# Optimization experiments

Hardware: AMD Instinct MI355X
Metric: run time of the kernel (lower is better)

## Reference

```python
import jax, jax.numpy as jnp
import numpy as np
from jax import lax

WINDOW_SIZE = 11
GAUSSIAN_SIGMA = 1.5
CROP_BORDER = 4
C1 = (0.01 * 255.0) ** 2
C2 = (0.03 * 255.0) ** 2


def _gaussian_kernel_window(ws: int, sigma: float) -> jnp.ndarray:
    # matches cv2.getGaussianKernel(ws, sigma) outer product
    x = jnp.arange(ws, dtype=jnp.float32) - (ws - 1) / 2.0
    g = jnp.exp(-(x ** 2) / (2.0 * sigma ** 2))
    g = g / jnp.sum(g)
    return jnp.outer(g, g)  # [ws, ws]


def _depthwise_conv(x: jnp.ndarray, kern: jnp.ndarray) -> jnp.ndarray:
    # x: [N, C, H, W]; kern: [C, 1, ws, ws]; valid padding, stride 1, groups=C
    return lax.conv_general_dilated(
        x, kern, window_strides=(1, 1), padding='VALID',
        dimension_numbers=('NCHW', 'OIHW', 'NCHW'),
        feature_group_count=x.shape[1])


def setup_inputs() -> dict:
    key = jax.random.key(0)
    k1, k2 = jax.random.split(key)
    raw_tensor = jax.random.uniform(k1, (32, 3, 512, 512), dtype=jnp.float32)
    dst_tensor = jax.random.uniform(k2, (32, 3, 512, 512), dtype=jnp.float32)
    return {"raw_tensor": raw_tensor, "dst_tensor": dst_tensor}


def reference(raw_tensor, dst_tensor):
    cb = CROP_BORDER
    raw = raw_tensor[:, :, cb:-cb, cb:-cb] * 255.0
    dst = dst_tensor[:, :, cb:-cb, cb:-cb] * 255.0
    C = raw.shape[1]
    kern = jnp.broadcast_to(
        _gaussian_kernel_window(WINDOW_SIZE, GAUSSIAN_SIGMA)[None, None],
        (C, 1, WINDOW_SIZE, WINDOW_SIZE)).astype(raw.dtype)

    raw_mean = _depthwise_conv(raw, kern)
    dst_mean = _depthwise_conv(dst, kern)
    raw_mean_sq = raw_mean ** 2
    dst_mean_sq = dst_mean ** 2
    raw_dst_mean = raw_mean * dst_mean
    raw_var = _depthwise_conv(raw * raw, kern) - raw_mean_sq
    dst_var = _depthwise_conv(dst * dst, kern) - dst_mean_sq
    raw_dst_cov = _depthwise_conv(raw * dst, kern) - raw_dst_mean

    num = (2.0 * raw_dst_mean + C1) * (2.0 * raw_dst_cov + C2)
    den = (raw_mean_sq + dst_mean_sq + C1) * (raw_var + dst_var + C2)
    ssim_map = num / den
    return jnp.mean(ssim_map, axis=(1, 2, 3)).astype(jnp.float32)  # [B]
```

## Files before the change

### kernel.cpp

```cpp
#include <hip/hip_runtime.h>


#define IMG   512
#define OUTD  494
#define CB    4
#define TW    64
#define TH    26
#define VSW   76
#define C1F   6.5025f
#define C2F   58.5225f
#define NPIX  732108.0f
#define XBLK  8
#define YBLK  19
#define SLOTS 456

__global__ __launch_bounds__(256, 4) void ssim_main(
        const float* __restrict__ raw, const float* __restrict__ dst,
        float* __restrict__ partial) {
    __shared__ float vs[4][TH][VSW];
    __shared__ float red[4];

    const int tid = threadIdx.x;
    const int bc  = blockIdx.z;
    const int b   = bc / 3;
    const int c3  = bc - b * 3;
    const int ty0 = blockIdx.y * TH;
    const int tx0 = blockIdx.x * TW;

    float gw[11];
    {
        float s = 0.f;
        #pragma unroll
        for (int k = 0; k < 11; ++k) {
            float x = (float)(k - 5);
            gw[k] = expf(-x * x * (1.0f / 4.5f));
            s += gw[k];
        }
        float inv = 1.0f / s;
        #pragma unroll
        for (int k = 0; k < 11; ++k) gw[k] *= inv;
    }

    const float* rb = raw + (size_t)bc * (IMG * IMG);
    const float* db = dst + (size_t)bc * (IMG * IMG);

    if (tid < 247) {
        const int rp = tid / 19;
        const int xg = tid - rp * 19;
        int col0 = CB + tx0 + xg * 4;
        if (col0 > IMG - 4) col0 = IMG - 4;
        const int row0 = CB + ty0 + rp * 2;

        float a0[4][4] = {{0.f}};
        float a1[4][4] = {{0.f}};
        #pragma unroll
        for (int k = 0; k < 12; ++k) {
            const int r = row0 + k;
            const float4 va = *(const float4*)(rb + (size_t)r * IMG + col0);
            const float4 vc = *(const float4*)(db + (size_t)r * IMG + col0);
            const float R[4] = {va.x, va.y, va.z, va.w};
            const float D[4] = {vc.x, vc.y, vc.z, vc.w};
            float s2[4], p2[4];
            #pragma unroll
            for (int c = 0; c < 4; ++c) {
                const float u = R[c] + D[c];
                s2[c] = fmaf(R[c], R[c], D[c] * D[c]);
                p2[c] = u * u;
            }
            if (k < 11) {
                const float w = gw[k];
                #pragma unroll
                for (int c = 0; c < 4; ++c) {
                    a0[0][c] = fmaf(w, R[c],  a0[0][c]);
                    a0[1][c] = fmaf(w, D[c],  a0[1][c]);
                    a0[2][c] = fmaf(w, s2[c], a0[2][c]);
                    a0[3][c] = fmaf(w, p2[c], a0[3][c]);
                }
            }
            if (k >= 1) {
                const float w = gw[k - 1];
                #pragma unroll
                for (int c = 0; c < 4; ++c) {
                    a1[0][c] = fmaf(w, R[c],  a1[0][c]);
                    a1[1][c] = fmaf(w, D[c],  a1[1][c]);
                    a1[2][c] = fmaf(w, s2[c], a1[2][c]);
                    a1[3][c] = fmaf(w, p2[c], a1[3][c]);
                }
            }
        }
        #pragma unroll
        for (int f = 0; f < 4; ++f) {
            *(float4*)&vs[f][rp * 2 + 0][xg * 4] =
                make_float4(a0[f][0], a0[f][1], a0[f][2], a0[f][3]);
            *(float4*)&vs[f][rp * 2 + 1][xg * 4] =
                make_float4(a1[f][0], a1[f][1], a1[f][2], a1[f][3]);
        }
    }
    __syncthreads();

    const int row = tid & 31;
    const int xg  = tid >> 5;
    const int ox0 = tx0 + xg * 8;

    float ssum = 0.f;
    if (row < TH) {
        float m[4][8];
        #pragma unroll
        for (int f = 0; f < 4; ++f) {
            const float4* vp = (const float4*)&vs[f][row][xg * 8];
            const float4 A = vp[0], B = vp[1], Cq = vp[2], Dq = vp[3], Eq = vp[4];
            const float win[20] = {A.x, A.y, A.z, A.w,  B.x, B.y, B.z, B.w,
                                   Cq.x, Cq.y, Cq.z, Cq.w, Dq.x, Dq.y, Dq.z, Dq.w,
                                   Eq.x, Eq.y, Eq.z, Eq.w};
            #pragma unroll
            for (int c = 0; c < 8; ++c) {
                float o = 0.f;
                #pragma unroll
                for (int k = 0; k < 11; ++k) o = fmaf(gw[k], win[c + k], o);
                m[f][c] = o;
            }
        }
        #pragma unroll
        for (int c = 0; c < 8; ++c) {
            if (ox0 + c < OUTD) {
                const float mr  = m[0][c] * 255.0f;
                const float md  = m[1][c] * 255.0f;
                const float S2  = m[2][c] * 65025.0f;
                const float P2  = m[3][c] * 65025.0f;
                const float mr2 = mr * mr, md2 = md * md, mpr = mr * md;
                const float num = (2.0f * mpr + C1F) *
                                  ((P2 - S2) - 2.0f * mpr + C2F);
                const float den = (mr2 + md2 + C1F) *
                                  ((S2 - mr2 - md2) + C2F);
                ssum = fmaf(num, __builtin_amdgcn_rcpf(den), ssum);
            }
        }
    }

    #pragma unroll
    for (int off = 32; off > 0; off >>= 1)
        ssum += __shfl_down(ssum, off, 64);
    const int lane = tid & 63, wv = tid >> 6;
    if (lane == 0) red[wv] = ssum;
    __syncthreads();
    if (tid == 0) {
        const float t = red[0] + red[1] + red[2] + red[3];
        partial[(size_t)b * SLOTS + (blockIdx.y * gridDim.x + blockIdx.x) * 3 + c3] = t;
    }
}

__global__ __launch_bounds__(128) void ssim_final(
        const float* __restrict__ partial, float* __restrict__ out) {
    __shared__ float red[2];
    const int b = blockIdx.x, tid = threadIdx.x;
    float s = 0.f;
    for (int i = tid; i < SLOTS; i += 128) s += partial[(size_t)b * SLOTS + i];
    #pragma unroll
    for (int off = 32; off > 0; off >>= 1) s += __shfl_down(s, off, 64);
    if ((tid & 63) == 0) red[tid >> 6] = s;
    __syncthreads();
    if (tid == 0) out[b] = (red[0] + red[1]) * (1.0f / NPIX);
}

extern "C" void kernel_launch(void* const* d_in, const int* in_sizes, int n_in,
                              void* d_out, int out_size, void* d_ws, size_t ws_size,
                              hipStream_t stream) {
    const float* raw = (const float*)d_in[0];
    const float* dst = (const float*)d_in[1];
    float* out     = (float*)d_out;
    float* partial = (float*)d_ws;

    dim3 grid(XBLK, YBLK, 96);
    ssim_main<<<grid, 256, 0, stream>>>(raw, dst, partial);
    ssim_final<<<32, 128, 0, stream>>>(partial, out);
}
```

Baseline: 276.5 us.

## Exploit Gaussian symmetry, narrow vertical pass to float2, and interleave horizontal convolutions

The 11 Gaussian weights are now stored as 6 symmetric values, and the horizontal pass adds the mirrored samples before multiplying, which saves about half the FMAs. The vertical pass now gives each thread 2 columns and loops over 494 work items, so all 256 threads take part instead of 247 threads each doing 4 columns. The horizontal convolutions are reordered to run one feature at a time and fold into the SSIM terms as they go, which shortens register live ranges. The costs are more global load instructions per byte from float2 loads and a second loop iteration for some threads.

Result: no change. 279.0 us (+0.9%).

```diff
diff --git a/kernel.cpp b/kernel.cpp
--- a/kernel.cpp
+++ b/kernel.cpp
@@ -14,6 +14,8 @@
 #define YBLK  19
 #define SLOTS 456
 
+#define GW(k) g[(k) <= 5 ? (k) : 10 - (k)]
+
 __global__ __launch_bounds__(256, 4) void ssim_main(
         const float* __restrict__ raw, const float* __restrict__ dst,
         float* __restrict__ partial) {
@@ -27,50 +29,51 @@
     const int ty0 = blockIdx.y * TH;
     const int tx0 = blockIdx.x * TW;
 
-    float gw[11];
+    float g[6];
     {
-        float s = 0.f;
+        float t[6];
         #pragma unroll
-        for (int k = 0; k < 11; ++k) {
-            float x = (float)(k - 5);
-            gw[k] = expf(-x * x * (1.0f / 4.5f));
-            s += gw[k];
+        for (int k = 0; k < 6; ++k) {
+            const float x = (float)(k - 5);
+            t[k] = expf(-x * x * (1.0f / 4.5f));
         }
-        float inv = 1.0f / s;
+        const float s = 2.f * (t[0] + t[1] + t[2] + t[3] + t[4]) + t[5];
+        const float inv = 1.0f / s;
         #pragma unroll
-        for (int k = 0; k < 11; ++k) gw[k] *= inv;
+        for (int k = 0; k < 6; ++k) g[k] = t[k] * inv;
     }
 
     const float* rb = raw + (size_t)bc * (IMG * IMG);
     const float* db = dst + (size_t)bc * (IMG * IMG);
 
-    if (tid < 247) {
-        const int rp = tid / 19;
-        const int xg = tid - rp * 19;
-        int col0 = CB + tx0 + xg * 4;
-        if (col0 > IMG - 4) col0 = IMG - 4;
+    #pragma unroll 1
+    for (int t = tid; t < 494; t += 256) {
+        const int rp = t / 38;
+        const int xg = t - rp * 38;
+        int col0 = CB + tx0 + xg * 2;
+        if (col0 > IMG - 2) col0 = IMG - 2;
         const int row0 = CB + ty0 + rp * 2;
 
-        float a0[4][4] = {{0.f}};
-        float a1[4][4] = {{0.f}};
+        float a0[4][2] = {{0.f}};
+        float a1[4][2] = {{0.f}};
         #pragma unroll
         for (int k = 0; k < 12; ++k) {
             const int r = row0 + k;
-            const float4 va = *(const float4*)(rb + (size_t)r * IMG + col0);
-            const float4 vc = *(const float4*)(db + (size_t)r * IMG + col0);
-            const float R[4] = {va.x, va.y, va.z, va.w};
-            const float D[4] = {vc.x, vc.y, vc.z, vc.w};
-            float s2[4], p2[4];
+            const float2 va = *(const float2*)(rb + (size_t)r * IMG + col0);
+            const float2 vc = *(const float2*)(db + (size_t)r * IMG + col0);
+            const float R[2] = {va.x, va.y};
+            const float D[2] = {vc.x, vc.y};
+            float s2[2], p2[2];
             #pragma unroll
-            for (int c = 0; c < 4; ++c) {
+            for (int c = 0; c < 2; ++c) {
                 const float u = R[c] + D[c];
                 s2[c] = fmaf(R[c], R[c], D[c] * D[c]);
                 p2[c] = u * u;
             }
             if (k < 11) {
-                const float w = gw[k];
+                const float w = GW(k);
                 #pragma unroll
-                for (int c = 0; c < 4; ++c) {
+                for (int c = 0; c < 2; ++c) {
                     a0[0][c] = fmaf(w, R[c],  a0[0][c]);
                     a0[1][c] = fmaf(w, D[c],  a0[1][c]);
                     a0[2][c] = fmaf(w, s2[c], a0[2][c]);
@@ -78,9 +81,9 @@
                 }
             }
             if (k >= 1) {
-                const float w = gw[k - 1];
+                const float w = GW(k - 1);
                 #pragma unroll
-                for (int c = 0; c < 4; ++c) {
+                for (int c = 0; c < 2; ++c) {
                     a1[0][c] = fmaf(w, R[c],  a1[0][c]);
                     a1[1][c] = fmaf(w, D[c],  a1[1][c]);
                     a1[2][c] = fmaf(w, s2[c], a1[2][c]);
@@ -90,10 +93,8 @@
         }
         #pragma unroll
         for (int f = 0; f < 4; ++f) {
-            *(float4*)&vs[f][rp * 2 + 0][xg * 4] =
-                make_float4(a0[f][0], a0[f][1], a0[f][2], a0[f][3]);
-            *(float4*)&vs[f][rp * 2 + 1][xg * 4] =
-                make_float4(a1[f][0], a1[f][1], a1[f][2], a1[f][3]);
+            *(float2*)&vs[f][rp * 2 + 0][xg * 2] = make_float2(a0[f][0], a0[f][1]);
+            *(float2*)&vs[f][rp * 2 + 1][xg * 2] = make_float2(a1[f][0], a1[f][1]);
         }
     }
     __syncthreads();
@@ -102,37 +103,54 @@
     const int xg  = tid >> 5;
     const int ox0 = tx0 + xg * 8;
 
+    #define HCONV(f, o)                                                      \
+    {                                                                        \
+        const float4* vp = (const float4*)&vs[f][row][xg * 8];               \
+        const float4 A = vp[0], B = vp[1], Cq = vp[2], Dq = vp[3];           \
+        const float2 E2 = *(const float2*)&vs[f][row][xg * 8 + 16];          \
+        const float w_[18] = {A.x, A.y, A.z, A.w,  B.x, B.y, B.z, B.w,       \
+                              Cq.x, Cq.y, Cq.z, Cq.w, Dq.x, Dq.y, Dq.z, Dq.w,\
+                              E2.x, E2.y};                                   \
+        _Pragma("unroll")                                                    \
+        for (int c = 0; c < 8; ++c) {                                        \
+            float t5 = g[5] * w_[c + 5];                                     \
+            _Pragma("unroll")                                                \
+            for (int j = 0; j < 5; ++j)                                      \
+                t5 = fmaf(g[j], w_[c + j] + w_[c + 10 - j], t5);             \
+            o[c] = t5;                                                       \
+        }                                                                    \
+    }
+
     float ssum = 0.f;
     if (row < TH) {
-        float m[4][8];
+        float m0[8], m1[8];
+        HCONV(0, m0);
+        HCONV(1, m1);
+        float q1[8], q2[8];
         #pragma unroll
-        for (int f = 0; f < 4; ++f) {
-            const float4* vp = (const float4*)&vs[f][row][xg * 8];
-            const float4 A = vp[0], B = vp[1], Cq = vp[2], Dq = vp[3], Eq = vp[4];
-            const float win[20] = {A.x, A.y, A.z, A.w,  B.x, B.y, B.z, B.w,
-                                   Cq.x, Cq.y, Cq.z, Cq.w, Dq.x, Dq.y, Dq.z, Dq.w,
-                                   Eq.x, Eq.y, Eq.z, Eq.w};
-            #pragma unroll
-            for (int c = 0; c < 8; ++c) {
-                float o = 0.f;
-                #pragma unroll
-                for (int k = 0; k < 11; ++k) o = fmaf(gw[k], win[c + k], o);
-                m[f][c] = o;
-            }
+        for (int c = 0; c < 8; ++c) {
+            const float a = m0[c] * 255.0f;
+            const float d = m1[c] * 255.0f;
+            q1[c] = fmaf(a, a, d * d);
+            q2[c] = a * d;
         }
+        float S2[8];
+        HCONV(2, S2);
+        float den[8];
+        #pragma unroll
+        for (int c = 0; c < 8; ++c) {
+            S2[c] *= 65025.0f;
+            den[c] = (q1[c] + C1F) * ((S2[c] - q1[c]) + C2F);
+        }
+        float P2[8];
+        HCONV(3, P2);
         #pragma unroll
         for (int c = 0; c < 8; ++c) {
             if (ox0 + c < OUTD) {
-                const float mr  = m[0][c] * 255.0f;
-                const float md  = m[1][c] * 255.0f;
-                const float S2  = m[2][c] * 65025.0f;
-                const float P2  = m[3][c] * 65025.0f;
-                const float mr2 = mr * mr, md2 = md * md, mpr = mr * md;
-                const float num = (2.0f * mpr + C1F) *
-                                  ((P2 - S2) - 2.0f * mpr + C2F);
-                const float den = (mr2 + md2 + C1F) *
-                                  ((S2 - mr2 - md2) + C2F);
-                ssum = fmaf(num, __builtin_amdgcn_rcpf(den), ssum);
+                const float P   = P2[c] * 65025.0f;
+                const float num = fmaf(2.0f, q2[c], C1F) *
+                                  ((P - S2[c]) - 2.0f * q2[c] + C2F);
+                ssum = fmaf(num, __builtin_amdgcn_rcpf(den[c]), ssum);
             }
         }
     }
```
